# Performance work log

Hardware: AMD Instinct MI355X
Metric: run time of the kernel (lower is better)

## Reference

```python
import jax, jax.numpy as jnp
import numpy as np

N = 50000
E = 1600000
F_IN = 128
MP_UNITS = [32, 32, 32, 32, 16, 16, 16, 16, 8, 8, 8, 8]
MLP_UNITS = [16, 16]
DELTA = 2.0


def _lin(k, fi, fo):
    kw, kb = jax.random.split(k)
    s = 1.0 / np.sqrt(fi)
    W = jax.random.uniform(kw, (fi, fo), minval=-s, maxval=s, dtype=jnp.float32)
    b = jax.random.uniform(kb, (fo,), minval=-s, maxval=s, dtype=jnp.float32)
    return W, b


def setup_inputs() -> dict:
    key = jax.random.key(0)
    ks = jax.random.split(key, 64)
    inp = {}
    inp['x'] = jax.random.normal(ks[0], (N, F_IN), dtype=jnp.float32)
    inp['edge_index'] = jax.random.randint(ks[1], (2, E), 0, N, dtype=jnp.int32)
    inp['edge_weight'] = jax.random.uniform(ks[2], (E,), dtype=jnp.float32)
    inp['Wi'], inp['bi'] = _lin(ks[3], F_IN, F_IN)
    d = F_IN
    for i, u in enumerate(MP_UNITS):
        inp['Wc%d' % i], inp['bc%d' % i] = _lin(ks[4 + i], d, u)
        d = u
    for i, u in enumerate(MLP_UNITS):
        inp['Wm%d' % i], inp['bm%d' % i] = _lin(ks[20 + i], d, u)
        d = u
    inp['Wf'], inp['bf'] = _lin(ks[30], d, 1)
    return inp


def reference(x, edge_index, edge_weight, Wi, bi,
              Wc0, bc0, Wc1, bc1, Wc2, bc2, Wc3, bc3, Wc4, bc4, Wc5, bc5,
              Wc6, bc6, Wc7, bc7, Wc8, bc8, Wc9, bc9, Wc10, bc10, Wc11, bc11,
              Wm0, bm0, Wm1, bm1, Wf, bf):
    n = x.shape[0]
    src, dst = edge_index[0], edge_index[1]
    # delta_gcn_matrix: P = (1-delta) I + delta * D^{-1/2} A D^{-1/2}
    deg = jax.ops.segment_sum(edge_weight, dst, num_segments=n)
    dinv = jnp.where(deg > 0, jax.lax.rsqrt(jnp.maximum(deg, 1e-12)), 0.0)
    w = DELTA * dinv[src] * edge_weight * dinv[dst]  # [E]
    self_w = 1.0 - DELTA

    h = x @ Wi + bi

    def conv(h, W, b):
        hw = h @ W                                        # [N, out]
        msg = hw[src] * w[:, None]                        # gather + scale [E, out]
        agg = jax.ops.segment_sum(msg, dst, num_segments=n)  # scatter-add
        return agg + self_w * hw + b                      # fold in self-loops

    convs = [(Wc0, bc0), (Wc1, bc1), (Wc2, bc2), (Wc3, bc3), (Wc4, bc4), (Wc5, bc5),
             (Wc6, bc6), (Wc7, bc7), (Wc8, bc8), (Wc9, bc9), (Wc10, bc10), (Wc11, bc11)]
    for W, b in convs:
        h = jnp.tanh(conv(h, W, b))
    for W, b in [(Wm0, bm0), (Wm1, bm1)]:
        h = jax.nn.relu(h @ W + b)
    return jnp.tanh(h @ Wf + bf)  # [N, 1]
```

## Files before the change

### kernel.cpp

```cpp
#include <hip/hip_runtime.h>


constexpr int kN = 50000;
constexpr int kE = 1600000;
constexpr float kSelfW = -1.0f;
constexpr int kCAP = 72;
constexpr int PAD_N = 50176;
constexpr int kPROWS = PAD_N / 8;
constexpr int E4  = kE / 4;
constexpr int E8B = (E4 + 511) / 512;
constexpr int NBG = (kN + 255) / 256;

typedef int      v4i __attribute__((ext_vector_type(4)));
typedef float    v4f __attribute__((ext_vector_type(4)));
typedef _Float16 h8v __attribute__((ext_vector_type(8)));

__device__ __forceinline__ int rowmap(int r) {
  return (r & 7) * kPROWS + (r >> 3);
}
__device__ __forceinline__ unsigned packcw(int colMapped, float w) {
  _Float16 h = (_Float16)w;
  unsigned short u;
  __builtin_memcpy(&u, &h, 2);
  return (unsigned)(unsigned short)colMapped | ((unsigned)u << 16);
}
__device__ __forceinline__ float unpw(unsigned e) {
  unsigned short u = (unsigned short)(e >> 16);
  _Float16 h;
  __builtin_memcpy(&h, &u, 2);
  return (float)h;
}
__device__ __forceinline__ unsigned pack2h(float a, float b) {
  _Float16 ha = (_Float16)a, hb = (_Float16)b;
  unsigned short ua, ub;
  __builtin_memcpy(&ua, &ha, 2);
  __builtin_memcpy(&ub, &hb, 2);
  return (unsigned)ua | ((unsigned)ub << 16);
}
__device__ __forceinline__ float fast_tanh(float x) {
  float t = __expf(2.0f * x);
  float r = __builtin_amdgcn_rcpf(t + 1.0f);
  return 1.0f - 2.0f * r;
}

__global__ __launch_bounds__(256)
void prep(int* __restrict__ cnt, const float* __restrict__ Wi,
          const float* __restrict__ bi, const float* __restrict__ Wc0,
          float* __restrict__ Weff, float* __restrict__ beff) {
  if (blockIdx.x < 49) {
    int i = blockIdx.x * 1024 + threadIdx.x * 4;
    *reinterpret_cast<int4*>(cnt + i) = make_int4(0, 0, 0, 0);
  } else {
    int idx = (blockIdx.x - 49) * 256 + threadIdx.x;
    if (idx >= 129 * 32) return;
    int r = idx >> 5, j = idx & 31;
    float acc = 0.0f;
    if (r < 128) {
      for (int k = 0; k < 128; ++k) acc += Wi[r * 128 + k] * Wc0[k * 32 + j];
      Weff[r * 32 + j] = acc;
    } else {
      for (int k = 0; k < 128; ++k) acc += bi[k] * Wc0[k * 32 + j];
      beff[j] = acc;
    }
  }
}

__global__ __launch_bounds__(256)
void build_cnt_gemm0(const int* __restrict__ src, const int* __restrict__ dst,
                     const float* __restrict__ ew, int* __restrict__ cnt,
                     unsigned* __restrict__ ecw,
                     const float* __restrict__ X,
                     const float* __restrict__ Weff,
                     const float* __restrict__ beff,
                     _Float16* __restrict__ Y, int e4, int n) {
  __shared__ unsigned s_buf[4128];
  if (blockIdx.x < NBG) {
    float* smem = reinterpret_cast<float*>(s_buf);
    for (int idx = threadIdx.x; idx < 128 * 32; idx += 256) {
      int j = idx >> 7, k = idx & 127;
      smem[j * 128 + k] = Weff[k * 32 + j];
    }
    if (threadIdx.x < 32) smem[4096 + threadIdx.x] = beff[threadIdx.x];
    __syncthreads();
    int row = blockIdx.x * 256 + threadIdx.x;
    if (row >= n) return;
    float acc[32];
#pragma unroll
    for (int j = 0; j < 32; ++j) acc[j] = smem[4096 + j];
    const float4* xr = reinterpret_cast<const float4*>(X + (size_t)row * 128);
    const float4* Ws4 = reinterpret_cast<const float4*>(smem);
    for (int k4 = 0; k4 < 32; ++k4) {
      float4 a = xr[k4];
#pragma unroll
      for (int j = 0; j < 32; ++j) {
        float4 wv = Ws4[j * 32 + k4];
        acc[j] += a.x * wv.x + a.y * wv.y + a.z * wv.z + a.w * wv.w;
      }
    }
    h8v* yr = reinterpret_cast<h8v*>(Y + (size_t)rowmap(row) * 32);
#pragma unroll
    for (int j8 = 0; j8 < 4; ++j8) {
      h8v v;
#pragma unroll
      for (int q = 0; q < 8; ++q) v[q] = (_Float16)acc[8 * j8 + q];
      yr[j8] = v;
    }
    return;
  }
  unsigned*       s_cw = s_buf;
  unsigned short* s_br = reinterpret_cast<unsigned short*>(s_buf + 2048);
  int*            s_cnt = reinterpret_cast<int*>(s_buf + 3072);
  if (threadIdx.x == 0) *s_cnt = 0;
  __syncthreads();
  int b = blockIdx.x - NBG;
  int p = blockIdx.x & 7;
  int chunk = b >> 3;
  int lane = threadIdx.x & 63;
  int i0 = chunk * 512 + threadIdx.x;
  int i1 = i0 + 256;
  v4i svA = {0,0,0,0}, dvA = {-1,-1,-1,-1};
  v4i svB = {0,0,0,0}, dvB = {-1,-1,-1,-1};
  v4f wvA = {0,0,0,0}, wvB = {0,0,0,0};
  bool vA = i0 < e4, vB = i1 < e4;
  if (vA) {
    svA = reinterpret_cast<const v4i*>(src)[i0];
    dvA = reinterpret_cast<const v4i*>(dst)[i0];
    wvA = reinterpret_cast<const v4f*>(ew)[i0];
  }
  if (vB) {
    svB = reinterpret_cast<const v4i*>(src)[i1];
    dvB = reinterpret_cast<const v4i*>(dst)[i1];
    wvB = reinterpret_cast<const v4f*>(ew)[i1];
  }
#pragma unroll
  for (int g = 0; g < 2; ++g) {
    v4i sv = g ? svB : svA;
    v4i dv = g ? dvB : dvA;
    v4f wv = g ? wvB : wvA;
    bool valid = g ? vB : vA;
#pragma unroll
    for (int c = 0; c < 4; ++c) {
      bool keep = valid && ((dv[c] & 7) == p);
      unsigned long long mask = __ballot(keep);
      int base = 0;
      int nb = __popcll(mask);
      if (lane == 0 && nb) base = atomicAdd(s_cnt, nb);
      base = __shfl(base, 0, 64);
      if (keep) {
        int pos = base + __popcll(mask & ((1ull << lane) - 1ull));
        s_cw[pos] = packcw(rowmap(sv[c]), wv[c]);
        s_br[pos] = (unsigned short)(dv[c] >> 3);
      }
    }
  }
  __syncthreads();
  int m = *s_cnt;
  for (int t = threadIdx.x; t < m; t += 256) {
    int br = p * kPROWS + s_br[t];
    int r = atomicAdd(&cnt[br], 1);
    if (r < kCAP) ecw[(size_t)br * kCAP + r] = s_cw[t];
  }
}

__global__ __launch_bounds__(256)
void deg_dinv_wave(const int* __restrict__ cnt, const unsigned* __restrict__ ecw,
                   float* __restrict__ dinv) {
  int lane = threadIdx.x & 63;
  int br = blockIdx.x * 4 + (threadIdx.x >> 6);
  int deg = min(cnt[br], kCAP);
  size_t base = (size_t)br * kCAP;
  float d = 0.0f;
  for (int i = lane; i < deg; i += 64) d += unpw(ecw[base + i]);
#pragma unroll
  for (int off = 32; off > 0; off >>= 1) d += __shfl_xor(d, off, 64);
  if (lane == 0) dinv[br] = (d > 0.0f) ? rsqrtf(fmaxf(d, 1e-12f)) : 0.0f;
}

__global__ __launch_bounds__(256)
void wscale_wave(const int* __restrict__ cnt, unsigned* __restrict__ ecw,
                 const float* __restrict__ dinv) {
  int lane = threadIdx.x & 63;
  int br = blockIdx.x * 4 + (threadIdx.x >> 6);
  int deg = min(cnt[br], kCAP);
  size_t base = (size_t)br * kCAP;
  float dr = 2.0f * dinv[br];
  for (int i = lane; i < kCAP; i += 64) {
    if (i < deg) {
      unsigned e = ecw[base + i];
      int cm = e & 0xFFFFu;
      ecw[base + i] = packcw(cm, dr * dinv[cm] * unpw(e));
    } else {
      ecw[base + i] = 0u;
    }
  }
}

template <int DOUT, int DNEXT, bool FINAL>
__global__ __launch_bounds__(256)
void spmm_fused(const _Float16* __restrict__ HW, const int* __restrict__ cnt,
                const unsigned* __restrict__ ecw, const float* __restrict__ b,
                const float* __restrict__ Wn, void* __restrict__ Out,
                const float* __restrict__ Wm0, const float* __restrict__ bm0,
                const float* __restrict__ Wm1, const float* __restrict__ bm1,
                const float* __restrict__ Wf, const float* __restrict__ bf,
                int n) {
  constexpr int R = 64 / DOUT;
  constexpr int W = DOUT;
  constexpr int L = DOUT / 8;
  constexpr int S = 8;
  constexpr int WST = DNEXT + 1;
  constexpr int JPT = (DNEXT > 0) ? (DNEXT / S) : 1;
  __shared__ float smem[(DNEXT > 0) ? DOUT * WST : 448];
  if constexpr (DNEXT > 0) {
    for (int idx = threadIdx.x; idx < DOUT * DNEXT; idx += 256) {
      int k = idx / DNEXT, j = idx - k * DNEXT;
      smem[k * WST + j] = Wn[idx];
    }
    __syncthreads();
  }
  if constexpr (FINAL) {
    int t = threadIdx.x;
    if (t < 128) smem[t] = Wm0[t];
    if (t < 256) smem[128 + t] = Wm1[t];
    if (t < 16) {
      smem[384 + t] = bm0[t];
      smem[400 + t] = bm1[t];
      smem[416 + t] = Wf[t];
    }
    if (t == 0) smem[432] = bf[0];
    __syncthreads();
  }
  int lane = threadIdx.x & 63;
  int wid = threadIdx.x >> 6;
  int g = lane / W;
  int gl = lane - g * W;
  int ch8 = gl & (L - 1);
  int sub = gl / L;
  int p = blockIdx.x & 7;
  int q = blockIdx.x >> 3;
  int brLocal = q * (4 * R) + wid * R + g;
  int br = p * kPROWS + brLocal;
  int deg = min(cnt[br], kCAP);
  const uint4* ecw4 = reinterpret_cast<const uint4*>(ecw + (size_t)br * kCAP);
  const h8v* HW8 = reinterpret_cast<const h8v*>(HW);
  uint4 ea = ecw4[sub];
  uint4 eb = ecw4[8 + sub];
  h8v a0 = HW8[(size_t)(ea.x & 0xFFFFu) * L + ch8];
  h8v a1 = HW8[(size_t)(ea.y & 0xFFFFu) * L + ch8];
  h8v a2 = HW8[(size_t)(ea.z & 0xFFFFu) * L + ch8];
  h8v a3 = HW8[(size_t)(ea.w & 0xFFFFu) * L + ch8];
  h8v b0 = HW8[(size_t)(eb.x & 0xFFFFu) * L + ch8];
  h8v b1 = HW8[(size_t)(eb.y & 0xFFFFu) * L + ch8];
  h8v b2 = HW8[(size_t)(eb.z & 0xFFFFu) * L + ch8];
  h8v b3 = HW8[(size_t)(eb.w & 0xFFFFu) * L + ch8];
  float wa0 = unpw(ea.x), wa1 = unpw(ea.y), wa2 = unpw(ea.z), wa3 = unpw(ea.w);
  float wb0 = unpw(eb.x), wb1 = unpw(eb.y), wb2 = unpw(eb.z), wb3 = unpw(eb.w);
  float acc[8];
#pragma unroll
  for (int q8 = 0; q8 < 8; ++q8)
    acc[q8] = wa0 * (float)a0[q8] + wa1 * (float)a1[q8] +
              wa2 * (float)a2[q8] + wa3 * (float)a3[q8] +
              wb0 * (float)b0[q8] + wb1 * (float)b1[q8] +
              wb2 * (float)b2[q8] + wb3 * (float)b3[q8];
  if (deg > 64) {
    if (sub < 2) {
      uint4 et = ecw4[16 + sub];
      h8v t0 = HW8[(size_t)(et.x & 0xFFFFu) * L + ch8];
      h8v t1 = HW8[(size_t)(et.y & 0xFFFFu) * L + ch8];
      h8v t2 = HW8[(size_t)(et.z & 0xFFFFu) * L + ch8];
      h8v t3 = HW8[(size_t)(et.w & 0xFFFFu) * L + ch8];
      float u0 = unpw(et.x), u1 = unpw(et.y), u2 = unpw(et.z), u3 = unpw(et.w);
#pragma unroll
      for (int q8 = 0; q8 < 8; ++q8)
        acc[q8] += u0 * (float)t0[q8] + u1 * (float)t1[q8] +
                   u2 * (float)t2[q8] + u3 * (float)t3[q8];
    }
  }
#pragma unroll
  for (int off = W / 2; off >= L; off >>= 1) {
#pragma unroll
    for (int q8 = 0; q8 < 8; ++q8) acc[q8] += __shfl_xor(acc[q8], off, 64);
  }
  int krow = 8 * ch8;
  h8v hsv = HW8[(size_t)br * L + ch8];
  float h[8];
#pragma unroll
  for (int q8 = 0; q8 < 8; ++q8)
    h[q8] = fast_tanh(acc[q8] + kSelfW * (float)hsv[q8] + b[krow + q8]);
  if constexpr (FINAL) {
    int row = (brLocal << 3) | p;
    if (gl == 0 && row < n) {
      float y0[16];
#pragma unroll
      for (int j = 0; j < 16; ++j) {
        float v = smem[384 + j];
#pragma unroll
        for (int k = 0; k < 8; ++k) v += h[k] * smem[k * 16 + j];
        y0[j] = fmaxf(v, 0.0f);
      }
      float y1[16];
#pragma unroll
      for (int j = 0; j < 16; ++j) {
        float v = smem[400 + j];
#pragma unroll
        for (int k = 0; k < 16; ++k) v += y0[k] * smem[128 + k * 16 + j];
        y1[j] = fmaxf(v, 0.0f);
      }
      float z = smem[432];
#pragma unroll
      for (int k = 0; k < 16; ++k) z += y1[k] * smem[416 + k];
      reinterpret_cast<float*>(Out)[row] = fast_tanh(z);
    }
  } else {
    float pj[JPT];
    int jbase = sub * JPT;
#pragma unroll
    for (int jj = 0; jj < JPT; ++jj) {
      int j = jbase + jj;
      float v = 0.0f;
#pragma unroll
      for (int q8 = 0; q8 < 8; ++q8) v += h[q8] * smem[(krow + q8) * WST + j];
      pj[jj] = v;
    }
#pragma unroll
    for (int off = 1; off < L; off <<= 1) {
#pragma unroll
      for (int jj = 0; jj < JPT; ++jj) pj[jj] += __shfl_xor(pj[jj], off, 64);
    }
    if (ch8 == 0) {
      _Float16* op = reinterpret_cast<_Float16*>(Out) + (size_t)br * DNEXT + jbase;
      if constexpr (JPT == 4) {
        uint2 u = make_uint2(pack2h(pj[0], pj[1]), pack2h(pj[2], pj[3]));
        *reinterpret_cast<uint2*>(op) = u;
      } else if constexpr (JPT == 2) {
        *reinterpret_cast<unsigned*>(op) = pack2h(pj[0], pj[1]);
      } else {
        op[0] = (_Float16)pj[0];
      }
    }
  }
}

extern "C" void kernel_launch(void* const* d_in, const int* in_sizes, int n_in,
                              void* d_out, int out_size, void* d_ws, size_t ws_size,
                              hipStream_t stream) {
  const float* x   = (const float*)d_in[0];
  const int*  eidx = (const int*)d_in[1];
  const float* ew  = (const float*)d_in[2];
  const float* Wi  = (const float*)d_in[3];
  const float* bi  = (const float*)d_in[4];
  const float* Wc[12]; const float* bc[12];
  for (int i = 0; i < 12; ++i) {
    Wc[i] = (const float*)d_in[5 + 2 * i];
    bc[i] = (const float*)d_in[6 + 2 * i];
  }
  const float* Wm0 = (const float*)d_in[29]; const float* bm0 = (const float*)d_in[30];
  const float* Wm1 = (const float*)d_in[31]; const float* bm1 = (const float*)d_in[32];
  const float* Wf  = (const float*)d_in[33]; const float* bf  = (const float*)d_in[34];
  float* out = (float*)d_out;

  const int* src = eidx;
  const int* dst = eidx + kE;

  float* wsf = (float*)d_ws;
  size_t off = 0;
  float*     dinv = wsf + off;              off += PAD_N;
  float*     Weff = wsf + off;              off += 128 * 32;
  float*     beff = wsf + off;              off += 64;
  int*       cnt  = (int*)(wsf + off);      off += PAD_N;
  unsigned*  ecw  = (unsigned*)(wsf + off); off += (size_t)PAD_N * kCAP;
  _Float16*  B16  = (_Float16*)(wsf + off); off += (size_t)PAD_N * 16;
  _Float16*  C16  = (_Float16*)(wsf + off); off += (size_t)PAD_N * 16;

  const int dgb  = PAD_N / 4;
  const int sb32 = PAD_N / 8;
  const int sb16 = PAD_N / 16;
  const int sb8  = PAD_N / 32;

  prep<<<66, 256, 0, stream>>>(cnt, Wi, bi, Wc[0], Weff, beff);
  build_cnt_gemm0<<<NBG + 8 * E8B, 256, 0, stream>>>(src, dst, ew, cnt, ecw,
                                                     x, Weff, beff, B16, E4, kN);
  deg_dinv_wave<<<dgb, 256, 0, stream>>>(cnt, ecw, dinv);
  wscale_wave<<<dgb, 256, 0, stream>>>(cnt, ecw, dinv);

  spmm_fused<32, 32, false><<<sb32, 256, 0, stream>>>(B16, cnt, ecw, bc[0], Wc[1], C16, nullptr, nullptr, nullptr, nullptr, nullptr, nullptr, kN);
  spmm_fused<32, 32, false><<<sb32, 256, 0, stream>>>(C16, cnt, ecw, bc[1], Wc[2], B16, nullptr, nullptr, nullptr, nullptr, nullptr, nullptr, kN);
  spmm_fused<32, 32, false><<<sb32, 256, 0, stream>>>(B16, cnt, ecw, bc[2], Wc[3], C16, nullptr, nullptr, nullptr, nullptr, nullptr, nullptr, kN);
  spmm_fused<32, 16, false><<<sb32, 256, 0, stream>>>(C16, cnt, ecw, bc[3], Wc[4], B16, nullptr, nullptr, nullptr, nullptr, nullptr, nullptr, kN);
  spmm_fused<16, 16, false><<<sb16, 256, 0, stream>>>(B16, cnt, ecw, bc[4], Wc[5], C16, nullptr, nullptr, nullptr, nullptr, nullptr, nullptr, kN);
  spmm_fused<16, 16, false><<<sb16, 256, 0, stream>>>(C16, cnt, ecw, bc[5], Wc[6], B16, nullptr, nullptr, nullptr, nullptr, nullptr, nullptr, kN);
  spmm_fused<16, 16, false><<<sb16, 256, 0, stream>>>(B16, cnt, ecw, bc[6], Wc[7], C16, nullptr, nullptr, nullptr, nullptr, nullptr, nullptr, kN);
  spmm_fused<16, 8, false><<<sb16, 256, 0, stream>>>(C16, cnt, ecw, bc[7], Wc[8], B16, nullptr, nullptr, nullptr, nullptr, nullptr, nullptr, kN);
  spmm_fused<8, 8, false><<<sb8, 256, 0, stream>>>(B16, cnt, ecw, bc[8], Wc[9], C16, nullptr, nullptr, nullptr, nullptr, nullptr, nullptr, kN);
  spmm_fused<8, 8, false><<<sb8, 256, 0, stream>>>(C16, cnt, ecw, bc[9], Wc[10], B16, nullptr, nullptr, nullptr, nullptr, nullptr, nullptr, kN);
  spmm_fused<8, 8, false><<<sb8, 256, 0, stream>>>(B16, cnt, ecw, bc[10], Wc[11], C16, nullptr, nullptr, nullptr, nullptr, nullptr, nullptr, kN);
  spmm_fused<8, 0, true><<<sb8, 256, 0, stream>>>(C16, cnt, ecw, bc[11], nullptr, out, Wm0, bm0, Wm1, bm1, Wf, bf, kN);
}
```

Baseline: 455.0 us.

## Fuse all graph phases into one persistent cooperative kernel with grid syncs

Replaces the sequence of fifteen separate kernel launches (build, degree, weight scaling, twelve SpMM layers) with a single cooperative persistent kernel that loops over work items and uses grid-wide barriers between phases. The aim is to remove per-launch overhead and launch gaps between the many small layers. A grid-stride fallback path with separate kernels is kept for when cooperative launch fails. The trade-offs are grid-sync cost, a grid capped at 1536 blocks, and an occupancy hint of 4 blocks per CU that may constrain registers in the heavy build/GEMM phase.

```diff
diff --git a/kernel.cpp b/kernel.cpp
--- a/kernel.cpp
+++ b/kernel.cpp
@@ -1,5 +1,8 @@
 #include <hip/hip_runtime.h>
-
+#include <hip/hip_cooperative_groups.h>
+
+
+namespace cg = cooperative_groups;
 
 constexpr int kN = 50000;
 constexpr int kE = 1600000;
@@ -10,10 +13,29 @@
 constexpr int E4  = kE / 4;
 constexpr int E8B = (E4 + 511) / 512;
 constexpr int NBG = (kN + 255) / 256;
+constexpr int NW_BUILD = NBG + 8 * E8B;
+constexpr int NW_DEG = PAD_N / 4;
+constexpr int SB32 = PAD_N / 8;
+constexpr int SB16 = PAD_N / 16;
+constexpr int SB8  = PAD_N / 32;
+constexpr int GRID_CAP = 1536;
+constexpr int kCUs = 256;
 
 typedef int      v4i __attribute__((ext_vector_type(4)));
 typedef float    v4f __attribute__((ext_vector_type(4)));
 typedef _Float16 h8v __attribute__((ext_vector_type(8)));
+
+struct MegaArgs {
+  const int* src; const int* dst; const float* ew;
+  int* cnt; unsigned* ecw;
+  const float* X; const float* Weff; const float* beff;
+  _Float16* B16; _Float16* C16;
+  float* dinv;
+  const float* bc[12]; const float* Wc[12];
+  const float* Wm0; const float* bm0; const float* Wm1; const float* bm1;
+  const float* Wf; const float* bf;
+  float* out;
+};
 
 __device__ __forceinline__ int rowmap(int r) {
   return (r & 7) * kPROWS + (r >> 3);
@@ -65,280 +87,316 @@
   }
 }
 
-__global__ __launch_bounds__(256)
-void build_cnt_gemm0(const int* __restrict__ src, const int* __restrict__ dst,
-                     const float* __restrict__ ew, int* __restrict__ cnt,
-                     unsigned* __restrict__ ecw,
-                     const float* __restrict__ X,
-                     const float* __restrict__ Weff,
-                     const float* __restrict__ beff,
-                     _Float16* __restrict__ Y, int e4, int n) {
-  __shared__ unsigned s_buf[4128];
-  if (blockIdx.x < NBG) {
-    float* smem = reinterpret_cast<float*>(s_buf);
-    for (int idx = threadIdx.x; idx < 128 * 32; idx += 256) {
-      int j = idx >> 7, k = idx & 127;
-      smem[j * 128 + k] = Weff[k * 32 + j];
-    }
-    if (threadIdx.x < 32) smem[4096 + threadIdx.x] = beff[threadIdx.x];
-    __syncthreads();
-    int row = blockIdx.x * 256 + threadIdx.x;
-    if (row >= n) return;
-    float acc[32];
-#pragma unroll
-    for (int j = 0; j < 32; ++j) acc[j] = smem[4096 + j];
-    const float4* xr = reinterpret_cast<const float4*>(X + (size_t)row * 128);
-    const float4* Ws4 = reinterpret_cast<const float4*>(smem);
-    for (int k4 = 0; k4 < 32; ++k4) {
-      float4 a = xr[k4];
-#pragma unroll
-      for (int j = 0; j < 32; ++j) {
-        float4 wv = Ws4[j * 32 + k4];
-        acc[j] += a.x * wv.x + a.y * wv.y + a.z * wv.z + a.w * wv.w;
-      }
-    }
-    h8v* yr = reinterpret_cast<h8v*>(Y + (size_t)rowmap(row) * 32);
-#pragma unroll
-    for (int j8 = 0; j8 < 4; ++j8) {
-      h8v v;
-#pragma unroll
-      for (int q = 0; q < 8; ++q) v[q] = (_Float16)acc[8 * j8 + q];
-      yr[j8] = v;
-    }
-    return;
-  }
-  unsigned*       s_cw = s_buf;
-  unsigned short* s_br = reinterpret_cast<unsigned short*>(s_buf + 2048);
-  int*            s_cnt = reinterpret_cast<int*>(s_buf + 3072);
-  if (threadIdx.x == 0) *s_cnt = 0;
-  __syncthreads();
-  int b = blockIdx.x - NBG;
-  int p = blockIdx.x & 7;
-  int chunk = b >> 3;
+__device__ __forceinline__ void build_phase(const MegaArgs& A, unsigned* s_buf,
+                                            int grid) {
+  for (int w = blockIdx.x; w < NW_BUILD; w += grid) {
+    if (w < NBG) {
+      float* smem = reinterpret_cast<float*>(s_buf);
+      for (int idx = threadIdx.x; idx < 128 * 32; idx += 256) {
+        int j = idx >> 7, k = idx & 127;
+        smem[j * 128 + k] = A.Weff[k * 32 + j];
+      }
+      if (threadIdx.x < 32) smem[4096 + threadIdx.x] = A.beff[threadIdx.x];
+      __syncthreads();
+      int row = w * 256 + threadIdx.x;
+      if (row < kN) {
+        float acc[32];
+#pragma unroll
+        for (int j = 0; j < 32; ++j) acc[j] = smem[4096 + j];
+        const float4* xr = reinterpret_cast<const float4*>(A.X + (size_t)row * 128);
+        const float4* Ws4 = reinterpret_cast<const float4*>(smem);
+        for (int k4 = 0; k4 < 32; ++k4) {
+          float4 a = xr[k4];
+#pragma unroll
+          for (int j = 0; j < 32; ++j) {
+            float4 wv = Ws4[j * 32 + k4];
+            acc[j] += a.x * wv.x + a.y * wv.y + a.z * wv.z + a.w * wv.w;
+          }
+        }
+        h8v* yr = reinterpret_cast<h8v*>(A.B16 + (size_t)rowmap(row) * 32);
+#pragma unroll
+        for (int j8 = 0; j8 < 4; ++j8) {
+          h8v v;
+#pragma unroll
+          for (int q = 0; q < 8; ++q) v[q] = (_Float16)acc[8 * j8 + q];
+          yr[j8] = v;
+        }
+      }
+      __syncthreads();
+    } else {
+      unsigned*       s_cw = s_buf;
+      unsigned short* s_br = reinterpret_cast<unsigned short*>(s_buf + 2048);
+      int*            s_cnt = reinterpret_cast<int*>(s_buf + 3072);
+      if (threadIdx.x == 0) *s_cnt = 0;
+      __syncthreads();
+      int p = w & 7;
+      int chunk = (w - NBG) >> 3;
+      int lane = threadIdx.x & 63;
+      int i0 = chunk * 512 + threadIdx.x;
+      int i1 = i0 + 256;
+      v4i svA = {0,0,0,0}, dvA = {-1,-1,-1,-1};
+      v4i svB = {0,0,0,0}, dvB = {-1,-1,-1,-1};
+      v4f wvA = {0,0,0,0}, wvB = {0,0,0,0};
+      bool vA = i0 < E4, vB = i1 < E4;
+      if (vA) {
+        svA = reinterpret_cast<const v4i*>(A.src)[i0];
+        dvA = reinterpret_cast<const v4i*>(A.dst)[i0];
+        wvA = reinterpret_cast<const v4f*>(A.ew)[i0];
+      }
+      if (vB) {
+        svB = reinterpret_cast<const v4i*>(A.src)[i1];
+        dvB = reinterpret_cast<const v4i*>(A.dst)[i1];
+        wvB = reinterpret_cast<const v4f*>(A.ew)[i1];
+      }
+#pragma unroll
+      for (int g = 0; g < 2; ++g) {
+        v4i sv = g ? svB : svA;
+        v4i dv = g ? dvB : dvA;
+        v4f wv = g ? wvB : wvA;
+        bool valid = g ? vB : vA;
+#pragma unroll
+        for (int c = 0; c < 4; ++c) {
+          bool keep = valid && ((dv[c] & 7) == p);
+          unsigned long long mask = __ballot(keep);
+          int base = 0;
+          int nb = __popcll(mask);
+          if (lane == 0 && nb) base = atomicAdd(s_cnt, nb);
+          base = __shfl(base, 0, 64);
+          if (keep) {
+            int pos = base + __popcll(mask & ((1ull << lane) - 1ull));
+            s_cw[pos] = packcw(rowmap(sv[c]), wv[c]);
+            s_br[pos] = (unsigned short)(dv[c] >> 3);
+          }
+        }
+      }
+      __syncthreads();
+      int m = *s_cnt;
+      for (int t = threadIdx.x; t < m; t += 256) {
+        int br = p * kPROWS + s_br[t];
+        int r = atomicAdd(&A.cnt[br], 1);
+        if (r < kCAP) A.ecw[(size_t)br * kCAP + r] = s_cw[t];
+      }
+      __syncthreads();
+    }
+  }
+}
+
+__device__ __forceinline__ void deg_phase(const MegaArgs& A, int grid) {
   int lane = threadIdx.x & 63;
-  int i0 = chunk * 512 + threadIdx.x;
-  int i1 = i0 + 256;
-  v4i svA = {0,0,0,0}, dvA = {-1,-1,-1,-1};
-  v4i svB = {0,0,0,0}, dvB = {-1,-1,-1,-1};
-  v4f wvA = {0,0,0,0}, wvB = {0,0,0,0};
-  bool vA = i0 < e4, vB = i1 < e4;
-  if (vA) {
-    svA = reinterpret_cast<const v4i*>(src)[i0];
-    dvA = reinterpret_cast<const v4i*>(dst)[i0];
-    wvA = reinterpret_cast<const v4f*>(ew)[i0];
-  }
-  if (vB) {
-    svB = reinterpret_cast<const v4i*>(src)[i1];
-    dvB = reinterpret_cast<const v4i*>(dst)[i1];
-    wvB = reinterpret_cast<const v4f*>(ew)[i1];
-  }
-#pragma unroll
-  for (int g = 0; g < 2; ++g) {
-    v4i sv = g ? svB : svA;
-    v4i dv = g ? dvB : dvA;
-    v4f wv = g ? wvB : wvA;
-    bool valid = g ? vB : vA;
-#pragma unroll
-    for (int c = 0; c < 4; ++c) {
-      bool keep = valid && ((dv[c] & 7) == p);
-      unsigned long long mask = __ballot(keep);
-      int base = 0;
-      int nb = __popcll(mask);
-      if (lane == 0 && nb) base = atomicAdd(s_cnt, nb);
-      base = __shfl(base, 0, 64);
-      if (keep) {
-        int pos = base + __popcll(mask & ((1ull << lane) - 1ull));
-        s_cw[pos] = packcw(rowmap(sv[c]), wv[c]);
-        s_br[pos] = (unsigned short)(dv[c] >> 3);
-      }
-    }
-  }
-  __syncthreads();
-  int m = *s_cnt;
-  for (int t = threadIdx.x; t < m; t += 256) {
-    int br = p * kPROWS + s_br[t];
-    int r = atomicAdd(&cnt[br], 1);
-    if (r < kCAP) ecw[(size_t)br * kCAP + r] = s_cw[t];
-  }
-}
-
-__global__ __launch_bounds__(256)
-void deg_dinv_wave(const int* __restrict__ cnt, const unsigned* __restrict__ ecw,
-                   float* __restrict__ dinv) {
+  int wid = threadIdx.x >> 6;
+  for (int w = blockIdx.x; w < NW_DEG; w += grid) {
+    int br = w * 4 + wid;
+    int deg = min(A.cnt[br], kCAP);
+    size_t base = (size_t)br * kCAP;
+    float d = 0.0f;
+    for (int i = lane; i < deg; i += 64) d += unpw(A.ecw[base + i]);
+#pragma unroll
+    for (int off = 32; off > 0; off >>= 1) d += __shfl_xor(d, off, 64);
+    if (lane == 0) A.dinv[br] = (d > 0.0f) ? rsqrtf(fmaxf(d, 1e-12f)) : 0.0f;
+  }
+}
+
+__device__ __forceinline__ void wscale_phase(const MegaArgs& A, int grid) {
   int lane = threadIdx.x & 63;
-  int br = blockIdx.x * 4 + (threadIdx.x >> 6);
-  int deg = min(cnt[br], kCAP);
-  size_t base = (size_t)br * kCAP;
-  float d = 0.0f;
-  for (int i = lane; i < deg; i += 64) d += unpw(ecw[base + i]);
-#pragma unroll
-  for (int off = 32; off > 0; off >>= 1) d += __shfl_xor(d, off, 64);
-  if (lane == 0) dinv[br] = (d > 0.0f) ? rsqrtf(fmaxf(d, 1e-12f)) : 0.0f;
-}
-
-__global__ __launch_bounds__(256)
-void wscale_wave(const int* __restrict__ cnt, unsigned* __restrict__ ecw,
-                 const float* __restrict__ dinv) {
-  int lane = threadIdx.x & 63;
-  int br = blockIdx.x * 4 + (threadIdx.x >> 6);
-  int deg = min(cnt[br], kCAP);
-  size_t base = (size_t)br * kCAP;
-  float dr = 2.0f * dinv[br];
-  for (int i = lane; i < kCAP; i += 64) {
-    if (i < deg) {
-      unsigned e = ecw[base + i];
-      int cm = e & 0xFFFFu;
-      ecw[base + i] = packcw(cm, dr * dinv[cm] * unpw(e));
-    } else {
-      ecw[base + i] = 0u;
+  int wid = threadIdx.x >> 6;
+  for (int w = blockIdx.x; w < NW_DEG; w += grid) {
+    int br = w * 4 + wid;
+    int deg = min(A.cnt[br], kCAP);
+    size_t base = (size_t)br * kCAP;
+    float dr = 2.0f * A.dinv[br];
+    for (int i = lane; i < kCAP; i += 64) {
+      if (i < deg) {
+        unsigned e = A.ecw[base + i];
+        int cm = e & 0xFFFFu;
+        A.ecw[base + i] = packcw(cm, dr * A.dinv[cm] * unpw(e));
+      } else {
+        A.ecw[base + i] = 0u;
+      }
     }
   }
 }
 
 template <int DOUT, int DNEXT, bool FINAL>
-__global__ __launch_bounds__(256)
-void spmm_fused(const _Float16* __restrict__ HW, const int* __restrict__ cnt,
-                const unsigned* __restrict__ ecw, const float* __restrict__ b,
-                const float* __restrict__ Wn, void* __restrict__ Out,
-                const float* __restrict__ Wm0, const float* __restrict__ bm0,
-                const float* __restrict__ Wm1, const float* __restrict__ bm1,
-                const float* __restrict__ Wf, const float* __restrict__ bf,
-                int n) {
+__device__ __forceinline__ void spmm_phase(const _Float16* HW, const float* b,
+                                           const float* Wn, void* Out,
+                                           const MegaArgs& A, float* smem,
+                                           int nwork, int grid) {
   constexpr int R = 64 / DOUT;
   constexpr int W = DOUT;
   constexpr int L = DOUT / 8;
   constexpr int S = 8;
   constexpr int WST = DNEXT + 1;
   constexpr int JPT = (DNEXT > 0) ? (DNEXT / S) : 1;
-  __shared__ float smem[(DNEXT > 0) ? DOUT * WST : 448];
   if constexpr (DNEXT > 0) {
     for (int idx = threadIdx.x; idx < DOUT * DNEXT; idx += 256) {
       int k = idx / DNEXT, j = idx - k * DNEXT;
       smem[k * WST + j] = Wn[idx];
     }
-    __syncthreads();
   }
   if constexpr (FINAL) {
     int t = threadIdx.x;
-    if (t < 128) smem[t] = Wm0[t];
-    if (t < 256) smem[128 + t] = Wm1[t];
+    if (t < 128) smem[t] = A.Wm0[t];
+    if (t < 256) smem[128 + t] = A.Wm1[t];
     if (t < 16) {
-      smem[384 + t] = bm0[t];
-      smem[400 + t] = bm1[t];
-      smem[416 + t] = Wf[t];
-    }
-    if (t == 0) smem[432] = bf[0];
-    __syncthreads();
-  }
+      smem[384 + t] = A.bm0[t];
+      smem[400 + t] = A.bm1[t];
+      smem[416 + t] = A.Wf[t];
+    }
+    if (t == 0) smem[432] = A.bf[0];
+  }
+  __syncthreads();
   int lane = threadIdx.x & 63;
   int wid = threadIdx.x >> 6;
   int g = lane / W;
   int gl = lane - g * W;
   int ch8 = gl & (L - 1);
   int sub = gl / L;
-  int p = blockIdx.x & 7;
-  int q = blockIdx.x >> 3;
-  int brLocal = q * (4 * R) + wid * R + g;
-  int br = p * kPROWS + brLocal;
-  int deg = min(cnt[br], kCAP);
-  const uint4* ecw4 = reinterpret_cast<const uint4*>(ecw + (size_t)br * kCAP);
   const h8v* HW8 = reinterpret_cast<const h8v*>(HW);
-  uint4 ea = ecw4[sub];
-  uint4 eb = ecw4[8 + sub];
-  h8v a0 = HW8[(size_t)(ea.x & 0xFFFFu) * L + ch8];
-  h8v a1 = HW8[(size_t)(ea.y & 0xFFFFu) * L + ch8];
-  h8v a2 = HW8[(size_t)(ea.z & 0xFFFFu) * L + ch8];
-  h8v a3 = HW8[(size_t)(ea.w & 0xFFFFu) * L + ch8];
-  h8v b0 = HW8[(size_t)(eb.x & 0xFFFFu) * L + ch8];
-  h8v b1 = HW8[(size_t)(eb.y & 0xFFFFu) * L + ch8];
-  h8v b2 = HW8[(size_t)(eb.z & 0xFFFFu) * L + ch8];
-  h8v b3 = HW8[(size_t)(eb.w & 0xFFFFu) * L + ch8];
-  float wa0 = unpw(ea.x), wa1 = unpw(ea.y), wa2 = unpw(ea.z), wa3 = unpw(ea.w);
-  float wb0 = unpw(eb.x), wb1 = unpw(eb.y), wb2 = unpw(eb.z), wb3 = unpw(eb.w);
-  float acc[8];
-#pragma unroll
-  for (int q8 = 0; q8 < 8; ++q8)
-    acc[q8] = wa0 * (float)a0[q8] + wa1 * (float)a1[q8] +
-              wa2 * (float)a2[q8] + wa3 * (float)a3[q8] +
-              wb0 * (float)b0[q8] + wb1 * (float)b1[q8] +
-              wb2 * (float)b2[q8] + wb3 * (float)b3[q8];
-  if (deg > 64) {
-    if (sub < 2) {
-      uint4 et = ecw4[16 + sub];
-      h8v t0 = HW8[(size_t)(et.x & 0xFFFFu) * L + ch8];
-      h8v t1 = HW8[(size_t)(et.y & 0xFFFFu) * L + ch8];
-      h8v t2 = HW8[(size_t)(et.z & 0xFFFFu) * L + ch8];
-      h8v t3 = HW8[(size_t)(et.w & 0xFFFFu) * L + ch8];
-      float u0 = unpw(et.x), u1 = unpw(et.y), u2 = unpw(et.z), u3 = unpw(et.w);
-#pragma unroll
-      for (int q8 = 0; q8 < 8; ++q8)
-        acc[q8] += u0 * (float)t0[q8] + u1 * (float)t1[q8] +
-                   u2 * (float)t2[q8] + u3 * (float)t3[q8];
-    }
-  }
-#pragma unroll
-  for (int off = W / 2; off >= L; off >>= 1) {
-#pragma unroll
-    for (int q8 = 0; q8 < 8; ++q8) acc[q8] += __shfl_xor(acc[q8], off, 64);
-  }
-  int krow = 8 * ch8;
-  h8v hsv = HW8[(size_t)br * L + ch8];
-  float h[8];
-#pragma unroll
-  for (int q8 = 0; q8 < 8; ++q8)
-    h[q8] = fast_tanh(acc[q8] + kSelfW * (float)hsv[q8] + b[krow + q8]);
-  if constexpr (FINAL) {
-    int row = (brLocal << 3) | p;
-    if (gl == 0 && row < n) {
-      float y0[16];
-#pragma unroll
-      for (int j = 0; j < 16; ++j) {
-        float v = smem[384 + j];
-#pragma unroll
-        for (int k = 0; k < 8; ++k) v += h[k] * smem[k * 16 + j];
-        y0[j] = fmaxf(v, 0.0f);
-      }
-      float y1[16];
-#pragma unroll
-      for (int j = 0; j < 16; ++j) {
-        float v = smem[400 + j];
-#pragma unroll
-        for (int k = 0; k < 16; ++k) v += y0[k] * smem[128 + k * 16 + j];
-        y1[j] = fmaxf(v, 0.0f);
-      }
-      float z = smem[432];
-#pragma unroll
-      for (int k = 0; k < 16; ++k) z += y1[k] * smem[416 + k];
-      reinterpret_cast<float*>(Out)[row] = fast_tanh(z);
-    }
-  } else {
-    float pj[JPT];
-    int jbase = sub * JPT;
-#pragma unroll
-    for (int jj = 0; jj < JPT; ++jj) {
-      int j = jbase + jj;
-      float v = 0.0f;
-#pragma unroll
-      for (int q8 = 0; q8 < 8; ++q8) v += h[q8] * smem[(krow + q8) * WST + j];
-      pj[jj] = v;
-    }
-#pragma unroll
-    for (int off = 1; off < L; off <<= 1) {
-#pragma unroll
-      for (int jj = 0; jj < JPT; ++jj) pj[jj] += __shfl_xor(pj[jj], off, 64);
-    }
-    if (ch8 == 0) {
-      _Float16* op = reinterpret_cast<_Float16*>(Out) + (size_t)br * DNEXT + jbase;
-      if constexpr (JPT == 4) {
-        uint2 u = make_uint2(pack2h(pj[0], pj[1]), pack2h(pj[2], pj[3]));
-        *reinterpret_cast<uint2*>(op) = u;
-      } else if constexpr (JPT == 2) {
-        *reinterpret_cast<unsigned*>(op) = pack2h(pj[0], pj[1]);
-      } else {
-        op[0] = (_Float16)pj[0];
-      }
-    }
-  }
+  for (int w = blockIdx.x; w < nwork; w += grid) {
+    int p = w & 7;
+    int q = w >> 3;
+    int brLocal = q * (4 * R) + wid * R + g;
+    int br = p * kPROWS + brLocal;
+    int deg = min(A.cnt[br], kCAP);
+    const uint4* ecw4 = reinterpret_cast<const uint4*>(A.ecw + (size_t)br * kCAP);
+    uint4 ea = ecw4[sub];
+    uint4 eb = ecw4[8 + sub];
+    h8v a0 = HW8[(size_t)(ea.x & 0xFFFFu) * L + ch8];
+    h8v a1 = HW8[(size_t)(ea.y & 0xFFFFu) * L + ch8];
+    h8v a2 = HW8[(size_t)(ea.z & 0xFFFFu) * L + ch8];
+    h8v a3 = HW8[(size_t)(ea.w & 0xFFFFu) * L + ch8];
+    h8v b0 = HW8[(size_t)(eb.x & 0xFFFFu) * L + ch8];
+    h8v b1 = HW8[(size_t)(eb.y & 0xFFFFu) * L + ch8];
+    h8v b2 = HW8[(size_t)(eb.z & 0xFFFFu) * L + ch8];
+    h8v b3 = HW8[(size_t)(eb.w & 0xFFFFu) * L + ch8];
+    float wa0 = unpw(ea.x), wa1 = unpw(ea.y), wa2 = unpw(ea.z), wa3 = unpw(ea.w);
+    float wb0 = unpw(eb.x), wb1 = unpw(eb.y), wb2 = unpw(eb.z), wb3 = unpw(eb.w);
+    float acc[8];
+#pragma unroll
+    for (int q8 = 0; q8 < 8; ++q8)
+      acc[q8] = wa0 * (float)a0[q8] + wa1 * (float)a1[q8] +
+                wa2 * (float)a2[q8] + wa3 * (float)a3[q8] +
+                wb0 * (float)b0[q8] + wb1 * (float)b1[q8] +
+                wb2 * (float)b2[q8] + wb3 * (float)b3[q8];
+    if (deg > 64) {
+      if (sub < 2) {
+        uint4 et = ecw4[16 + sub];
+        h8v t0 = HW8[(size_t)(et.x & 0xFFFFu) * L + ch8];
+        h8v t1 = HW8[(size_t)(et.y & 0xFFFFu) * L + ch8];
+        h8v t2 = HW8[(size_t)(et.z & 0xFFFFu) * L + ch8];
+        h8v t3 = HW8[(size_t)(et.w & 0xFFFFu) * L + ch8];
+        float u0 = unpw(et.x), u1 = unpw(et.y), u2 = unpw(et.z), u3 = unpw(et.w);
+#pragma unroll
+        for (int q8 = 0; q8 < 8; ++q8)
+          acc[q8] += u0 * (float)t0[q8] + u1 * (float)t1[q8] +
+                     u2 * (float)t2[q8] + u3 * (float)t3[q8];
+      }
+    }
+#pragma unroll
+    for (int off = W / 2; off >= L; off >>= 1) {
+#pragma unroll
+      for (int q8 = 0; q8 < 8; ++q8) acc[q8] += __shfl_xor(acc[q8], off, 64);
+    }
+    int krow = 8 * ch8;
+    h8v hsv = HW8[(size_t)br * L + ch8];
+    float h[8];
+#pragma unroll
+    for (int q8 = 0; q8 < 8; ++q8)
+      h[q8] = fast_tanh(acc[q8] + kSelfW * (float)hsv[q8] + b[krow + q8]);
+    if constexpr (FINAL) {
+      int row = (brLocal << 3) | p;
+      if (gl == 0 && row < kN) {
+        float y0[16];
+#pragma unroll
+        for (int j = 0; j < 16; ++j) {
+          float v = smem[384 + j];
+#pragma unroll
+          for (int k = 0; k < 8; ++k) v += h[k] * smem[k * 16 + j];
+          y0[j] = fmaxf(v, 0.0f);
+        }
+        float y1[16];
+#pragma unroll
+        for (int j = 0; j < 16; ++j) {
+          float v = smem[400 + j];
+#pragma unroll
+          for (int k = 0; k < 16; ++k) v += y0[k] * smem[128 + k * 16 + j];
+          y1[j] = fmaxf(v, 0.0f);
+        }
+        float z = smem[432];
+#pragma unroll
+        for (int k = 0; k < 16; ++k) z += y1[k] * smem[416 + k];
+        reinterpret_cast<float*>(Out)[row] = fast_tanh(z);
+      }
+    } else {
+      float pj[JPT];
+      int jbase = sub * JPT;
+#pragma unroll
+      for (int jj = 0; jj < JPT; ++jj) {
+        int j = jbase + jj;
+        float v = 0.0f;
+#pragma unroll
+        for (int q8 = 0; q8 < 8; ++q8) v += h[q8] * smem[(krow + q8) * WST + j];
+        pj[jj] = v;
+      }
+#pragma unroll
+      for (int off = 1; off < L; off <<= 1) {
+#pragma unroll
+        for (int jj = 0; jj < JPT; ++jj) pj[jj] += __shfl_xor(pj[jj], off, 64);
+      }
+      if (ch8 == 0) {
+        _Float16* op = reinterpret_cast<_Float16*>(Out) + (size_t)br * DNEXT + jbase;
+        if constexpr (JPT == 4) {
+          uint2 u = make_uint2(pack2h(pj[0], pj[1]), pack2h(pj[2], pj[3]));
+          *reinterpret_cast<uint2*>(op) = u;
+        } else if constexpr (JPT == 2) {
+          *reinterpret_cast<unsigned*>(op) = pack2h(pj[0], pj[1]);
+        } else {
+          op[0] = (_Float16)pj[0];
+        }
+      }
+    }
+  }
+}
+
+__global__ __launch_bounds__(256, 4)
+void mega(MegaArgs A) {
+  __shared__ unsigned s_buf[4128];
+  cg::grid_group gg = cg::this_grid();
+  float* smemF = reinterpret_cast<float*>(s_buf);
+  const int grid = gridDim.x;
+
+  build_phase(A, s_buf, grid);                                   gg.sync();
+  deg_phase(A, grid);                                            gg.sync();
+  wscale_phase(A, grid);                                         gg.sync();
+  spmm_phase<32, 32, false>(A.B16, A.bc[0], A.Wc[1], A.C16, A, smemF, SB32, grid); gg.sync();
+  spmm_phase<32, 32, false>(A.C16, A.bc[1], A.Wc[2], A.B16, A, smemF, SB32, grid); gg.sync();
+  spmm_phase<32, 32, false>(A.B16, A.bc[2], A.Wc[3], A.C16, A, smemF, SB32, grid); gg.sync();
+  spmm_phase<32, 16, false>(A.C16, A.bc[3], A.Wc[4], A.B16, A, smemF, SB32, grid); gg.sync();
+  spmm_phase<16, 16, false>(A.B16, A.bc[4], A.Wc[5], A.C16, A, smemF, SB16, grid); gg.sync();
+  spmm_phase<16, 16, false>(A.C16, A.bc[5], A.Wc[6], A.B16, A, smemF, SB16, grid); gg.sync();
+  spmm_phase<16, 16, false>(A.B16, A.bc[6], A.Wc[7], A.C16, A, smemF, SB16, grid); gg.sync();
+  spmm_phase<16,  8, false>(A.C16, A.bc[7], A.Wc[8], A.B16, A, smemF, SB16, grid); gg.sync();
+  spmm_phase<8,   8, false>(A.B16, A.bc[8], A.Wc[9], A.C16, A, smemF, SB8,  grid); gg.sync();
+  spmm_phase<8,   8, false>(A.C16, A.bc[9], A.Wc[10], A.B16, A, smemF, SB8, grid); gg.sync();
+  spmm_phase<8,   8, false>(A.B16, A.bc[10], A.Wc[11], A.C16, A, smemF, SB8, grid); gg.sync();
+  spmm_phase<8,   0, true >(A.C16, A.bc[11], nullptr, A.out, A, smemF, SB8, grid);
+}
+
+__global__ __launch_bounds__(256)
+void k_build(MegaArgs A) {
+  __shared__ unsigned s_buf[4128];
+  build_phase(A, s_buf, gridDim.x);
+}
+__global__ __launch_bounds__(256)
+void k_deg(MegaArgs A) { deg_phase(A, gridDim.x); }
+__global__ __launch_bounds__(256)
+void k_wscale(MegaArgs A) { wscale_phase(A, gridDim.x); }
+template <int DOUT, int DNEXT, bool FINAL>
+__global__ __launch_bounds__(256)
+void k_spmm(MegaArgs A, const _Float16* HW, const float* b,
+            const float* Wn, void* Out, int nwork) {
+  __shared__ float smem[4128];
+  spmm_phase<DOUT, DNEXT, FINAL>(HW, b, Wn, Out, A, smem, nwork, gridDim.x);
 }
 
 extern "C" void kernel_launch(void* const* d_in, const int* in_sizes, int n_in,
@@ -349,18 +407,6 @@
   const float* ew  = (const float*)d_in[2];
   const float* Wi  = (const float*)d_in[3];
   const float* bi  = (const float*)d_in[4];
-  const float* Wc[12]; const float* bc[12];
-  for (int i = 0; i < 12; ++i) {
-    Wc[i] = (const float*)d_in[5 + 2 * i];
-    bc[i] = (const float*)d_in[6 + 2 * i];
-  }
-  const float* Wm0 = (const float*)d_in[29]; const float* bm0 = (const float*)d_in[30];
-  const float* Wm1 = (const float*)d_in[31]; const float* bm1 = (const float*)d_in[32];
-  const float* Wf  = (const float*)d_in[33]; const float* bf  = (const float*)d_in[34];
-  float* out = (float*)d_out;
-
-  const int* src = eidx;
-  const int* dst = eidx + kE;
 
   float* wsf = (float*)d_ws;
   size_t off = 0;
@@ -372,27 +418,54 @@
   _Float16*  B16  = (_Float16*)(wsf + off); off += (size_t)PAD_N * 16;
   _Float16*  C16  = (_Float16*)(wsf + off); off += (size_t)PAD_N * 16;
 
-  const int dgb  = PAD_N / 4;
-  const int sb32 = PAD_N / 8;
-  const int sb16 = PAD_N / 16;
-  const int sb8  = PAD_N / 32;
-
-  prep<<<66, 256, 0, stream>>>(cnt, Wi, bi, Wc[0], Weff, beff);
-  build_cnt_gemm0<<<NBG + 8 * E8B, 256, 0, stream>>>(src, dst, ew, cnt, ecw,
-                                                     x, Weff, beff, B16, E4, kN);
-  deg_dinv_wave<<<dgb, 256, 0, stream>>>(cnt, ecw, dinv);
-  wscale_wave<<<dgb, 256, 0, stream>>>(cnt, ecw, dinv);
-
-  spmm_fused<32, 32, false><<<sb32, 256, 0, stream>>>(B16, cnt, ecw, bc[0], Wc[1], C16, nullptr, nullptr, nullptr, nullptr, nullptr, nullptr, kN);
-  spmm_fused<32, 32, false><<<sb32, 256, 0, stream>>>(C16, cnt, ecw, bc[1], Wc[2], B16, nullptr, nullptr, nullptr, nullptr, nullptr, nullptr, kN);
-  spmm_fused<32, 32, false><<<sb32, 256, 0, stream>>>(B16, cnt, ecw, bc[2], Wc[3], C16, nullptr, nullptr, nullptr, nullptr, nullptr, nullptr, kN);
-  spmm_fused<32, 16, false><<<sb32, 256, 0, stream>>>(C16, cnt, ecw, bc[3], Wc[4], B16, nullptr, nullptr, nullptr, nullptr, nullptr, nullptr, kN);
-  spmm_fused<16, 16, false><<<sb16, 256, 0, stream>>>(B16, cnt, ecw, bc[4], Wc[5], C16, nullptr, nullptr, nullptr, nullptr, nullptr, nullptr, kN);
-  spmm_fused<16, 16, false><<<sb16, 256, 0, stream>>>(C16, cnt, ecw, bc[5], Wc[6], B16, nullptr, nullptr, nullptr, nullptr, nullptr, nullptr, kN);
-  spmm_fused<16, 16, false><<<sb16, 256, 0, stream>>>(B16, cnt, ecw, bc[6], Wc[7], C16, nullptr, nullptr, nullptr, nullptr, nullptr, nullptr, kN);
-  spmm_fused<16, 8, false><<<sb16, 256, 0, stream>>>(C16, cnt, ecw, bc[7], Wc[8], B16, nullptr, nullptr, nullptr, nullptr, nullptr, nullptr, kN);
-  spmm_fused<8, 8, false><<<sb8, 256, 0, stream>>>(B16, cnt, ecw, bc[8], Wc[9], C16, nullptr, nullptr, nullptr, nullptr, nullptr, nullptr, kN);
-  spmm_fused<8, 8, false><<<sb8, 256, 0, stream>>>(C16, cnt, ecw, bc[9], Wc[10], B16, nullptr, nullptr, nullptr, nullptr, nullptr, nullptr, kN);
-  spmm_fused<8, 8, false><<<sb8, 256, 0, stream>>>(B16, cnt, ecw, bc[10], Wc[11], C16, nullptr, nullptr, nullptr, nullptr, nullptr, nullptr, kN);
-  spmm_fused<8, 0, true><<<sb8, 256, 0, stream>>>(C16, cnt, ecw, bc[11], nullptr, out, Wm0, bm0, Wm1, bm1, Wf, bf, kN);
-}
+  MegaArgs A;
+  A.src = eidx;
+  A.dst = eidx + kE;
+  A.ew  = ew;
+  A.cnt = cnt; A.ecw = ecw;
+  A.X = x; A.Weff = Weff; A.beff = beff;
+  A.B16 = B16; A.C16 = C16;
+  A.dinv = dinv;
+  for (int i = 0; i < 12; ++i) {
+    A.Wc[i] = (const float*)d_in[5 + 2 * i];
+    A.bc[i] = (const float*)d_in[6 + 2 * i];
+  }
+  A.Wm0 = (const float*)d_in[29]; A.bm0 = (const float*)d_in[30];
+  A.Wm1 = (const float*)d_in[31]; A.bm1 = (const float*)d_in[32];
+  A.Wf  = (const float*)d_in[33]; A.bf  = (const float*)d_in[34];
+  A.out = (float*)d_out;
+
+  prep<<<66, 256, 0, stream>>>(cnt, Wi, bi, (const float*)d_in[5], Weff, beff);
+
+  bool coop_ok = false;
+  int nb = 0;
+  if (hipOccupancyMaxActiveBlocksPerMultiprocessor(&nb, mega, 256, 0) ==
+          hipSuccess && nb > 0) {
+    int grid = nb * kCUs;
+    if (grid > GRID_CAP) grid = GRID_CAP;
+    grid &= ~7;
+    if (grid >= 8) {
+      void* kargs[] = { (void*)&A };
+      if (hipLaunchCooperativeKernel(mega, dim3(grid), dim3(256), kargs, 0,
+                                     stream) == hipSuccess)
+        coop_ok = true;
+    }
+  }
+  if (coop_ok) return;
+
+  k_build<<<NW_BUILD, 256, 0, stream>>>(A);
+  k_deg<<<NW_DEG, 256, 0, stream>>>(A);
+  k_wscale<<<NW_DEG, 256, 0, stream>>>(A);
+  k_spmm<32, 32, false><<<SB32, 256, 0, stream>>>(A, A.B16, A.bc[0], A.Wc[1], A.C16, SB32);
+  k_spmm<32, 32, false><<<SB32, 256, 0, stream>>>(A, A.C16, A.bc[1], A.Wc[2], A.B16, SB32);
+  k_spmm<32, 32, false><<<SB32, 256, 0, stream>>>(A, A.B16, A.bc[2], A.Wc[3], A.C16, SB32);
+  k_spmm<32, 16, false><<<SB32, 256, 0, stream>>>(A, A.C16, A.bc[3], A.Wc[4], A.B16, SB32);
+  k_spmm<16, 16, false><<<SB16, 256, 0, stream>>>(A, A.B16, A.bc[4], A.Wc[5], A.C16, SB16);
+  k_spmm<16, 16, false><<<SB16, 256, 0, stream>>>(A, A.C16, A.bc[5], A.Wc[6], A.B16, SB16);
+  k_spmm<16, 16, false><<<SB16, 256, 0, stream>>>(A, A.B16, A.bc[6], A.Wc[7], A.C16, SB16);
+  k_spmm<16,  8, false><<<SB16, 256, 0, stream>>>(A, A.C16, A.bc[7], A.Wc[8], A.B16, SB16);
+  k_spmm<8,   8, false><<<SB8, 256, 0, stream>>>(A, A.B16, A.bc[8], A.Wc[9], A.C16, SB8);
+  k_spmm<8,   8, false><<<SB8, 256, 0, stream>>>(A, A.C16, A.bc[9], A.Wc[10], A.B16, SB8);
+  k_spmm<8,   8, false><<<SB8, 256, 0, stream>>>(A, A.B16, A.bc[10], A.Wc[11], A.C16, SB8);
+  k_spmm<8,   0, true ><<<SB8, 256, 0, stream>>>(A, A.C16, A.bc[11], nullptr, A.out, SB8);
+}
```

New measurement: 1.512 ms. 232% more time.
